# Optimization experiments

Measured on AMD Instinct MI355X. Metric: run time of the kernel, lower is better.

Reference implementation:

```python
import jax, jax.numpy as jnp
import numpy as np

D_MODEL = 1024
N_HEADS = 16
D_K = D_MODEL // N_HEADS
NEG_INF = -1.0e9


def setup_inputs() -> dict:
    key = jax.random.key(0)
    ks = jax.random.split(key, 12)
    B, S = 2, 2048
    inp = {
        "q": jax.random.normal(ks[0], (B, S, D_MODEL), dtype=jnp.float32),
        "k": jax.random.normal(ks[1], (B, S, D_MODEL), dtype=jnp.float32),
        "v": jax.random.normal(ks[2], (B, S, D_MODEL), dtype=jnp.float32),
        "mask": jax.random.randint(ks[3], (B, 1, S, S), 0, 2, dtype=jnp.int32),
        "Wq": jax.random.normal(ks[4], (D_MODEL, D_MODEL), dtype=jnp.float32) / np.sqrt(D_MODEL),
        "bq": jnp.zeros((D_MODEL,), dtype=jnp.float32),
        "Wk": jax.random.normal(ks[5], (D_MODEL, D_MODEL), dtype=jnp.float32) / np.sqrt(D_MODEL),
        "bk": jnp.zeros((D_MODEL,), dtype=jnp.float32),
        "Wv": jax.random.normal(ks[6], (D_MODEL, D_MODEL), dtype=jnp.float32) / np.sqrt(D_MODEL),
        "bv": jnp.zeros((D_MODEL,), dtype=jnp.float32),
        "Wo": jax.random.normal(ks[7], (D_MODEL, D_MODEL), dtype=jnp.float32) / np.sqrt(D_MODEL),
        "bo": jnp.zeros((D_MODEL,), dtype=jnp.float32),
    }
    return inp


def _split_heads(x):
    B, S, _ = x.shape
    return x.reshape(B, S, N_HEADS, D_K).transpose(0, 2, 1, 3)  # [B,H,S,Dk]


def reference(q, k, v, mask, Wq, bq, Wk, bk, Wv, bv, Wo, bo):
    # QKV projections (nn.Linear: x @ W.T + b; here W stored as [in,out]-agnostic square)
    query = _split_heads(q @ Wq + bq)
    key_ = _split_heads(k @ Wk + bk)
    value = _split_heads(v @ Wv + bv)

    scale = 1.0 / np.sqrt(D_K).astype(np.float32)
    scores = jnp.einsum("bhqd,bhkd->bhqk", query, key_) * scale  # [B,H,S,S]
    scores = jnp.where(mask == 0, NEG_INF, scores)
    attn = jax.nn.softmax(scores, axis=-1)  # dropout is identity in eval (p=0.0)
    ctx = jnp.einsum("bhqk,bhkd->bhqd", attn, value)  # [B,H,S,Dk]

    B, H, S, Dk = ctx.shape
    ctx = ctx.transpose(0, 2, 1, 3).reshape(B, S, H * Dk)
    return ctx @ Wo + bo
```

## Files before the change

kernel.cpp:

```cpp
#include <hip/hip_runtime.h>
#include <hip/hip_bf16.h>

typedef __bf16 bf16_t;
typedef __bf16 bf16x2 __attribute__((ext_vector_type(2)));
typedef __bf16 bf16x8 __attribute__((ext_vector_type(8)));
typedef float f32x4 __attribute__((ext_vector_type(4)));
typedef float f32x16 __attribute__((ext_vector_type(16)));
typedef int intx4 __attribute__((ext_vector_type(4)));
typedef unsigned int u32;
typedef unsigned long long u64;

#define S_LEN 2048
#define DM 1024
#define NH 16
#define DK 64
#define M_ROWS 4096
#define SCALE_LOG2E 0.1803368801111204f

__device__ __forceinline__ int sw_off(int row, int col) {
  return row * 64 + ((((col >> 3) ^ row) & 7) << 3) + (col & 7);
}

__device__ __forceinline__ bf16x8 cvt8(const float4& a, const float4& b) {
  bf16x8 v;
  v[0] = (__bf16)a.x; v[1] = (__bf16)a.y; v[2] = (__bf16)a.z; v[3] = (__bf16)a.w;
  v[4] = (__bf16)b.x; v[5] = (__bf16)b.y; v[6] = (__bf16)b.z; v[7] = (__bf16)b.w;
  return v;
}

__device__ __forceinline__ void glds16(const bf16_t* g, bf16_t* l) {
  __builtin_amdgcn_global_load_lds(
      (const __attribute__((address_space(1))) void*)g,
      (__attribute__((address_space(3))) void*)l, 16, 0, 0);
}

__device__ __forceinline__ int pk2(float lo, float hi) {
  bf16x2 t;
  t[0] = (__bf16)lo;
  t[1] = (__bf16)hi;
  return __builtin_bit_cast(int, t);
}

__global__ __launch_bounds__(256) void pack_mask(
    const int* __restrict__ mask, u64* __restrict__ mb)
{
  const int g = blockIdx.x * 256 + threadIdx.x;
  const int q = g & 2047;
  const int kw = (g >> 11) & 31;
  const int b = g >> 16;
  const int* src = &mask[((size_t)(b * S_LEN + q)) * S_LEN + kw * 64];
  u64 bits = 0;
  #pragma unroll
  for (int i = 0; i < 16; ++i) {
    const int4 m4 = *(const int4*)&src[i * 4];
    bits |= (u64)(m4.x != 0) << (4 * i);
    bits |= (u64)(m4.y != 0) << (4 * i + 1);
    bits |= (u64)(m4.z != 0) << (4 * i + 2);
    bits |= (u64)(m4.w != 0) << (4 * i + 3);
  }
  mb[g] = bits;
}

__global__ __launch_bounds__(256) void cvt_inputs(
    const float* __restrict__ q, const float* __restrict__ k,
    const float* __restrict__ v, bf16_t* __restrict__ Xb)
{
  const int z = blockIdx.y;
  const float* __restrict__ src = (z == 0) ? q : ((z == 1) ? k : v);
  const size_t idx = ((size_t)blockIdx.x * 256 + threadIdx.x) * 8;
  const float4 a = *(const float4*)&src[idx];
  const float4 b = *(const float4*)&src[idx + 4];
  *(bf16x8*)&Xb[(size_t)z * M_ROWS * DM + idx] = cvt8(a, b);
}

__global__ __launch_bounds__(256) void transw_kernel(
    const float* __restrict__ Wq, const float* __restrict__ Wk,
    const float* __restrict__ Wv, const float* __restrict__ Wo,
    bf16_t* __restrict__ Wt)
{
  const int z = blockIdx.z;
  const float* __restrict__ W = (z == 0) ? Wq : ((z == 1) ? Wk : ((z == 2) ? Wv : Wo));
  bf16_t* __restrict__ out = Wt + (size_t)z * DM * DM;
  __shared__ float tile[64][65];
  const int tx = threadIdx.x & 31, ty = threadIdx.x >> 5;
  const int k0 = blockIdx.x * 64, n0 = blockIdx.y * 64;
  #pragma unroll
  for (int j = 0; j < 8; ++j) {
    const float2 v = *(const float2*)&W[(size_t)(k0 + ty + 8 * j) * DM + n0 + tx * 2];
    tile[ty + 8 * j][tx * 2] = v.x;
    tile[ty + 8 * j][tx * 2 + 1] = v.y;
  }
  __syncthreads();
  #pragma unroll
  for (int j = 0; j < 8; ++j) {
    const int a = ty + 8 * j;
    bf16x2 p;
    p[0] = (__bf16)tile[tx * 2][a];
    p[1] = (__bf16)tile[tx * 2 + 1][a];
    *(bf16x2*)&out[(size_t)(n0 + a) * DM + k0 + tx * 2] = p;
  }
}

__device__ __forceinline__ void gemm128_body(
    const bf16_t* __restrict__ A, const bf16_t* __restrict__ Bt,
    const float* __restrict__ bias, bf16_t* __restrict__ outb,
    float* __restrict__ outf)
{
  __shared__ __align__(16) bf16_t As[128 * 32];
  __shared__ __align__(16) bf16_t Bs[128 * 32];
  const int t = threadIdx.x, w = t >> 6, L = t & 63, quad = L >> 4, l16 = L & 15;
  const int m0 = blockIdx.x * 128, n0 = blockIdx.y * 128;
  const int mb = 64 * (w & 1), nb = 64 * (w >> 1);
  const int rowS = t >> 2, subS = (t & 3) * 8;

  f32x4 acc[4][4] = {};
  for (int k0 = 0; k0 < DM; k0 += 32) {
    __syncthreads();
    glds16(&A[(size_t)(m0 + rowS) * DM + k0 + subS],        &As[t * 8]);
    glds16(&A[(size_t)(m0 + 64 + rowS) * DM + k0 + subS],   &As[2048 + t * 8]);
    glds16(&Bt[(size_t)(n0 + rowS) * DM + k0 + subS],       &Bs[t * 8]);
    glds16(&Bt[(size_t)(n0 + 64 + rowS) * DM + k0 + subS],  &Bs[2048 + t * 8]);
    __syncthreads();
    bf16x8 af[4], bfr[4];
    #pragma unroll
    for (int mt = 0; mt < 4; ++mt)
      af[mt] = *(const bf16x8*)&As[(mb + 16 * mt + l16) * 32 + quad * 8];
    #pragma unroll
    for (int ct = 0; ct < 4; ++ct)
      bfr[ct] = *(const bf16x8*)&Bs[(nb + 16 * ct + l16) * 32 + quad * 8];
    #pragma unroll
    for (int mt = 0; mt < 4; ++mt)
      #pragma unroll
      for (int ct = 0; ct < 4; ++ct)
        acc[mt][ct] = __builtin_amdgcn_mfma_f32_16x16x32_bf16(af[mt], bfr[ct], acc[mt][ct], 0, 0, 0);
  }
  #pragma unroll
  for (int mt = 0; mt < 4; ++mt)
    #pragma unroll
    for (int ct = 0; ct < 4; ++ct)
      #pragma unroll
      for (int r = 0; r < 4; ++r) {
        const int row = m0 + mb + 16 * mt + quad * 4 + r;
        const int n = n0 + nb + 16 * ct + l16;
        const float val = acc[mt][ct][r] + bias[n];
        if (outb) outb[(size_t)row * DM + n] = (__bf16)val;
        else      outf[(size_t)row * DM + n] = val;
      }
}

__global__ __launch_bounds__(256) void gemm_qkv(
    const bf16_t* __restrict__ Xb, const bf16_t* __restrict__ Wt,
    const float* __restrict__ bq, const float* __restrict__ bk,
    const float* __restrict__ bv, bf16_t* __restrict__ QKVb)
{
  const int z = blockIdx.z;
  gemm128_body(Xb + (size_t)z * M_ROWS * DM, Wt + (size_t)z * DM * DM,
               (z == 0) ? bq : ((z == 1) ? bk : bv),
               QKVb + (size_t)z * M_ROWS * DM, nullptr);
}

__global__ __launch_bounds__(256) void gemm_out(
    const bf16_t* __restrict__ ctx, const bf16_t* __restrict__ Wto,
    const float* __restrict__ bo, float* __restrict__ out)
{
  gemm128_body(ctx, Wto, bo, nullptr, out);
}

__global__ __launch_bounds__(256) void transpV(
    const bf16_t* __restrict__ Vb, bf16_t* __restrict__ Vtw)
{
  __shared__ bf16_t Tr[64 * 72];
  const int t = threadIdx.x;
  const int key0 = blockIdx.x * 64;
  const int bh = blockIdx.y, b = bh >> 4, h = bh & 15;
  const int r = t >> 2, c = (t & 3) * 16;
  const bf16_t* src = &Vb[(size_t)(b * S_LEN + key0 + r) * DM + h * DK + c];
  const bf16x8 v0 = *(const bf16x8*)src;
  const bf16x8 v1 = *(const bf16x8*)(src + 8);
  #pragma unroll
  for (int j = 0; j < 8; ++j) {
    Tr[r * 72 + c + j] = v0[j];
    Tr[r * 72 + c + 8 + j] = v1[j];
  }
  __syncthreads();
  const int dv = t >> 2, kc = (t & 3) * 16;
  bf16_t ov[16];
  #pragma unroll
  for (int j = 0; j < 16; ++j) ov[j] = Tr[(kc + j) * 72 + dv];
  bf16_t* dst = &Vtw[((size_t)bh * DK + dv) * S_LEN + key0 + kc];
  *(bf16x8*)dst = *(bf16x8*)&ov[0];
  *(bf16x8*)(dst + 8) = *(bf16x8*)&ov[8];
}

__global__ __launch_bounds__(256, 2) void attn_kernel(
    const bf16_t* __restrict__ Qb, const bf16_t* __restrict__ Kb,
    const bf16_t* __restrict__ Vtw, const u64* __restrict__ mb,
    bf16_t* __restrict__ ctx)
{
  __shared__ __align__(16) bf16_t Qs[128 * 64];
  __shared__ __align__(16) bf16_t Ks[64 * 64];
  __shared__ __align__(16) bf16_t Vts[64 * 64];

  const int t = threadIdx.x, w = t >> 6, L = t & 63;
  const int l31 = L & 31, h5 = L >> 5;
  const int q0 = blockIdx.x * 128;
  const int bh = blockIdx.y, b = bh >> 4, h = bh & 15;
  const int sr = t >> 2, sc = (t & 3) * 16;

  #pragma unroll
  for (int half = 0; half < 2; ++half) {
    const int row = half * 64 + sr;
    const bf16_t* s = &Qb[(size_t)(b * S_LEN + q0 + row) * DM + h * DK + sc];
    *(bf16x8*)&Qs[sw_off(row, sc)]     = *(const bf16x8*)s;
    *(bf16x8*)&Qs[sw_off(row, sc + 8)] = *(const bf16x8*)(s + 8);
  }

  const int qg = q0 + 32 * w + l31;
  const u64* pm = &mb[(size_t)b * 32 * S_LEN + qg];
  const bf16_t* pk_src = &Kb[(size_t)(b * S_LEN + sr) * DM + h * DK + sc];
  const bf16_t* pv_src = &Vtw[((size_t)bh * DK + sr) * S_LEN + sc];

  bf16x8 kp0, kp1, vp0, vp1;
  u64 mp;
  kp0 = *(const bf16x8*)pk_src; kp1 = *(const bf16x8*)(pk_src + 8);
  vp0 = *(const bf16x8*)pv_src; vp1 = *(const bf16x8*)(pv_src + 8);
  mp = *pm;
  pk_src += (size_t)64 * DM; pv_src += 64; pm += S_LEN;

  f32x16 O[2] = {};
  float l_lane = 0.f;

  for (int kt = 0; kt < S_LEN / 64; ++kt) {
    __syncthreads();
    *(bf16x8*)&Ks[sw_off(sr, sc)]      = kp0;
    *(bf16x8*)&Ks[sw_off(sr, sc + 8)]  = kp1;
    *(bf16x8*)&Vts[sw_off(sr, sc)]     = vp0;
    *(bf16x8*)&Vts[sw_off(sr, sc + 8)] = vp1;
    const u64 mcur = mp;
    __syncthreads();

    if (kt + 1 < S_LEN / 64) {
      kp0 = *(const bf16x8*)pk_src; kp1 = *(const bf16x8*)(pk_src + 8);
      vp0 = *(const bf16x8*)pv_src; vp1 = *(const bf16x8*)(pv_src + 8);
      mp = *pm;
      pk_src += (size_t)64 * DM; pv_src += 64; pm += S_LEN;
    }

    f32x16 sacc[2] = {};
    #pragma unroll
    for (int ks = 0; ks < 4; ++ks) {
      const bf16x8 qf = *(const bf16x8*)&Qs[sw_off(32 * w + l31, ks * 16 + 8 * h5)];
      #pragma unroll
      for (int nt = 0; nt < 2; ++nt) {
        const bf16x8 kf = *(const bf16x8*)&Ks[sw_off(nt * 32 + l31, ks * 16 + 8 * h5)];
        sacc[nt] = __builtin_amdgcn_mfma_f32_32x32x16_bf16(kf, qf, sacc[nt], 0, 0, 0);
      }
    }

    const u32 mlo = ((u32)mcur) >> (4 * h5);
    const u32 mhi = ((u32)(mcur >> 32)) >> (4 * h5);
    #pragma unroll
    for (int nt = 0; nt < 2; ++nt) {
      const u32 mm = nt ? mhi : mlo;
      float p[16];
      #pragma unroll
      for (int r = 0; r < 16; ++r) {
        const int cb = (r & 3) + 8 * (r >> 2);
        float v = __builtin_exp2f(__builtin_fmaf(sacc[nt][r], SCALE_LOG2E, -16.f));
        v = ((mm >> cb) & 1u) ? v : 0.f;
        l_lane += v;
        p[r] = v;
      }
      #pragma unroll
      for (int ss = 0; ss < 2; ++ss) {
        const int x0 = pk2(p[8 * ss + 0], p[8 * ss + 1]);
        const int x1 = pk2(p[8 * ss + 2], p[8 * ss + 3]);
        const int y0 = pk2(p[8 * ss + 4], p[8 * ss + 5]);
        const int y1 = pk2(p[8 * ss + 6], p[8 * ss + 7]);
        const auto r0 = __builtin_amdgcn_permlane32_swap(x0, y0, false, false);
        const auto r1 = __builtin_amdgcn_permlane32_swap(x1, y1, false, false);
        intx4 wv;
        wv[0] = r0[0]; wv[1] = r1[0]; wv[2] = r0[1]; wv[3] = r1[1];
        const bf16x8 pf = __builtin_bit_cast(bf16x8, wv);
        const int s4 = 2 * nt + ss;
        #pragma unroll
        for (int ot = 0; ot < 2; ++ot) {
          const bf16x8 vf = *(const bf16x8*)&Vts[sw_off(32 * ot + l31, s4 * 16 + 8 * h5)];
          O[ot] = __builtin_amdgcn_mfma_f32_32x32x16_bf16(vf, pf, O[ot], 0, 0, 0);
        }
      }
    }
  }

  const float lsum = l_lane + __shfl_xor(l_lane, 32);
  const float inv = 1.f / lsum;
  __syncthreads();
  #pragma unroll
  for (int ot = 0; ot < 2; ++ot)
    #pragma unroll
    for (int r = 0; r < 16; ++r) {
      const int dv = 32 * ot + (r & 3) + 8 * (r >> 2) + 4 * h5;
      Qs[sw_off(32 * w + l31, dv)] = (__bf16)(O[ot][r] * inv);
    }
  const int erow = 32 * w + (L >> 1);
  const int ecol = (L & 1) * 32;
  bf16_t* dst = &ctx[(size_t)(b * S_LEN + q0 + erow) * DM + h * DK + ecol];
  #pragma unroll
  for (int c8 = 0; c8 < 4; ++c8)
    *(bf16x8*)(dst + 8 * c8) = *(const bf16x8*)&Qs[sw_off(erow, ecol + 8 * c8)];
}

extern "C" void kernel_launch(void* const* d_in, const int* in_sizes, int n_in,
                              void* d_out, int out_size, void* d_ws, size_t ws_size,
                              hipStream_t stream) {
  const float* q  = (const float*)d_in[0];
  const float* k  = (const float*)d_in[1];
  const float* v  = (const float*)d_in[2];
  const int* mask = (const int*)d_in[3];
  const float* Wq = (const float*)d_in[4];
  const float* bq = (const float*)d_in[5];
  const float* Wk = (const float*)d_in[6];
  const float* bk = (const float*)d_in[7];
  const float* Wv = (const float*)d_in[8];
  const float* bv = (const float*)d_in[9];
  const float* Wo = (const float*)d_in[10];
  const float* bo = (const float*)d_in[11];
  float* out = (float*)d_out;

  const size_t SLICE = (size_t)M_ROWS * DM;
  bf16_t* Xb   = (bf16_t*)d_ws;
  bf16_t* QKVb = Xb + 3 * SLICE;
  bf16_t* Wt   = QKVb + 3 * SLICE;
  u64* mbw     = (u64*)(Wt + (size_t)4 * DM * DM);
  bf16_t* ctx  = Xb;
  bf16_t* Vtw  = Xb + SLICE;

  pack_mask<<<dim3(512), dim3(256), 0, stream>>>(mask, mbw);
  cvt_inputs<<<dim3(2048, 3), dim3(256), 0, stream>>>(q, k, v, Xb);
  transw_kernel<<<dim3(16, 16, 4), dim3(256), 0, stream>>>(Wq, Wk, Wv, Wo, Wt);
  gemm_qkv<<<dim3(32, 8, 3), dim3(256), 0, stream>>>(Xb, Wt, bq, bk, bv, QKVb);
  transpV<<<dim3(32, 32), dim3(256), 0, stream>>>(QKVb + 2 * SLICE, Vtw);
  attn_kernel<<<dim3(16, 32), dim3(256), 0, stream>>>(QKVb, QKVb + SLICE, Vtw, mbw, ctx);
  gemm_out<<<dim3(32, 8), dim3(256), 0, stream>>>(ctx, Wt + (size_t)3 * DM * DM, bo, out);
}
```

Baseline: 281.5 us.

## Double-buffer attention K/V via async LDS loads and ballot-pack the mask

The attention kernel now stages K and V tiles straight into two LDS buffers with global_load_lds, so the next tile loads while the current one is being computed. This replaces the register-prefetch path and its two barriers per tile. Q fragments are hoisted into registers once, and s_setprio raises wave priority around the MFMA sections. The mask packer now reads one element per lane in a coalesced way and builds the 64-bit word with a wave ballot, using many more blocks. The cost is extra LDS for the second buffer, which may reduce occupancy, and the code relies on the compiler placing waits for the async LDS loads before each barrier.

```diff
diff --git a/kernel.cpp b/kernel.cpp
--- a/kernel.cpp
+++ b/kernel.cpp
@@ -44,21 +44,14 @@
 __global__ __launch_bounds__(256) void pack_mask(
     const int* __restrict__ mask, u64* __restrict__ mb)
 {
-  const int g = blockIdx.x * 256 + threadIdx.x;
-  const int q = g & 2047;
-  const int kw = (g >> 11) & 31;
-  const int b = g >> 16;
-  const int* src = &mask[((size_t)(b * S_LEN + q)) * S_LEN + kw * 64];
-  u64 bits = 0;
-  #pragma unroll
-  for (int i = 0; i < 16; ++i) {
-    const int4 m4 = *(const int4*)&src[i * 4];
-    bits |= (u64)(m4.x != 0) << (4 * i);
-    bits |= (u64)(m4.y != 0) << (4 * i + 1);
-    bits |= (u64)(m4.z != 0) << (4 * i + 2);
-    bits |= (u64)(m4.w != 0) << (4 * i + 3);
-  }
-  mb[g] = bits;
+  const int wgl = blockIdx.x * 4 + (threadIdx.x >> 6);
+  const int lane = threadIdx.x & 63;
+  const int q = wgl & 2047;
+  const int kw = (wgl >> 11) & 31;
+  const int b = wgl >> 16;
+  const int val = mask[((size_t)(b * S_LEN + q)) * S_LEN + kw * 64 + lane];
+  const u64 bits = __ballot(val != 0);
+  if (lane == 0) mb[wgl] = bits;
 }
 
 __global__ __launch_bounds__(256) void cvt_inputs(
@@ -198,8 +191,8 @@
     bf16_t* __restrict__ ctx)
 {
   __shared__ __align__(16) bf16_t Qs[128 * 64];
-  __shared__ __align__(16) bf16_t Ks[64 * 64];
-  __shared__ __align__(16) bf16_t Vts[64 * 64];
+  __shared__ __align__(16) bf16_t Ks[2][64 * 64];
+  __shared__ __align__(16) bf16_t Vts[2][64 * 64];
 
   const int t = threadIdx.x, w = t >> 6, L = t & 63;
   const int l31 = L & 31, h5 = L >> 5;
@@ -214,49 +207,48 @@
     *(bf16x8*)&Qs[sw_off(row, sc)]     = *(const bf16x8*)s;
     *(bf16x8*)&Qs[sw_off(row, sc + 8)] = *(const bf16x8*)(s + 8);
   }
+  __syncthreads();
+
+  bf16x8 qf[4];
+  #pragma unroll
+  for (int ks = 0; ks < 4; ++ks)
+    qf[ks] = *(const bf16x8*)&Qs[sw_off(32 * w + l31, ks * 16 + 8 * h5)];
+
+  const int ch = (L & 7) ^ (L >> 3);
+  const int row0 = w * 16 + (L >> 3);
+  const int kofs0 = w * 1024 + L * 8, kofs1 = kofs0 + 512;
+  const bf16_t* pK0 = &Kb[(size_t)(b * S_LEN + row0) * DM + h * DK + ch * 8];
+  const bf16_t* pK1 = pK0 + (size_t)8 * DM;
+  const bf16_t* pV0 = &Vtw[((size_t)bh * DK + row0) * S_LEN + ch * 8];
+  const bf16_t* pV1 = pV0 + (size_t)8 * S_LEN;
 
   const int qg = q0 + 32 * w + l31;
   const u64* pm = &mb[(size_t)b * 32 * S_LEN + qg];
-  const bf16_t* pk_src = &Kb[(size_t)(b * S_LEN + sr) * DM + h * DK + sc];
-  const bf16_t* pv_src = &Vtw[((size_t)bh * DK + sr) * S_LEN + sc];
-
-  bf16x8 kp0, kp1, vp0, vp1;
-  u64 mp;
-  kp0 = *(const bf16x8*)pk_src; kp1 = *(const bf16x8*)(pk_src + 8);
-  vp0 = *(const bf16x8*)pv_src; vp1 = *(const bf16x8*)(pv_src + 8);
-  mp = *pm;
-  pk_src += (size_t)64 * DM; pv_src += 64; pm += S_LEN;
+
+  auto stageKV = [&](int buf) {
+    glds16(pK0, &Ks[buf][kofs0]);
+    glds16(pK1, &Ks[buf][kofs1]);
+    glds16(pV0, &Vts[buf][kofs0]);
+    glds16(pV1, &Vts[buf][kofs1]);
+    pK0 += (size_t)64 * DM; pK1 += (size_t)64 * DM;
+    pV0 += 64; pV1 += 64;
+  };
 
   f32x16 O[2] = {};
   float l_lane = 0.f;
 
-  for (int kt = 0; kt < S_LEN / 64; ++kt) {
-    __syncthreads();
-    *(bf16x8*)&Ks[sw_off(sr, sc)]      = kp0;
-    *(bf16x8*)&Ks[sw_off(sr, sc + 8)]  = kp1;
-    *(bf16x8*)&Vts[sw_off(sr, sc)]     = vp0;
-    *(bf16x8*)&Vts[sw_off(sr, sc + 8)] = vp1;
-    const u64 mcur = mp;
-    __syncthreads();
-
-    if (kt + 1 < S_LEN / 64) {
-      kp0 = *(const bf16x8*)pk_src; kp1 = *(const bf16x8*)(pk_src + 8);
-      vp0 = *(const bf16x8*)pv_src; vp1 = *(const bf16x8*)(pv_src + 8);
-      mp = *pm;
-      pk_src += (size_t)64 * DM; pv_src += 64; pm += S_LEN;
-    }
-
+  auto compute = [&](const bf16_t* __restrict__ Kc, const bf16_t* __restrict__ Vc,
+                     u64 mcur) {
     f32x16 sacc[2] = {};
-    #pragma unroll
-    for (int ks = 0; ks < 4; ++ks) {
-      const bf16x8 qf = *(const bf16x8*)&Qs[sw_off(32 * w + l31, ks * 16 + 8 * h5)];
+    __builtin_amdgcn_s_setprio(1);
+    #pragma unroll
+    for (int ks = 0; ks < 4; ++ks)
       #pragma unroll
       for (int nt = 0; nt < 2; ++nt) {
-        const bf16x8 kf = *(const bf16x8*)&Ks[sw_off(nt * 32 + l31, ks * 16 + 8 * h5)];
-        sacc[nt] = __builtin_amdgcn_mfma_f32_32x32x16_bf16(kf, qf, sacc[nt], 0, 0, 0);
+        const bf16x8 kf = *(const bf16x8*)&Kc[sw_off(nt * 32 + l31, ks * 16 + 8 * h5)];
+        sacc[nt] = __builtin_amdgcn_mfma_f32_32x32x16_bf16(kf, qf[ks], sacc[nt], 0, 0, 0);
       }
-    }
-
+    __builtin_amdgcn_s_setprio(0);
     const u32 mlo = ((u32)mcur) >> (4 * h5);
     const u32 mhi = ((u32)(mcur >> 32)) >> (4 * h5);
     #pragma unroll
@@ -283,18 +275,39 @@
         wv[0] = r0[0]; wv[1] = r1[0]; wv[2] = r0[1]; wv[3] = r1[1];
         const bf16x8 pf = __builtin_bit_cast(bf16x8, wv);
         const int s4 = 2 * nt + ss;
+        __builtin_amdgcn_s_setprio(1);
         #pragma unroll
         for (int ot = 0; ot < 2; ++ot) {
-          const bf16x8 vf = *(const bf16x8*)&Vts[sw_off(32 * ot + l31, s4 * 16 + 8 * h5)];
+          const bf16x8 vf = *(const bf16x8*)&Vc[sw_off(32 * ot + l31, s4 * 16 + 8 * h5)];
           O[ot] = __builtin_amdgcn_mfma_f32_32x32x16_bf16(vf, pf, O[ot], 0, 0, 0);
         }
+        __builtin_amdgcn_s_setprio(0);
       }
     }
+  };
+
+  stageKV(0);
+  u64 mcur = *pm; pm += S_LEN;
+  u64 mnext;
+  __syncthreads();
+
+  for (int kt = 0; kt < S_LEN / 64; kt += 2) {
+    stageKV(1);
+    mnext = *pm; pm += S_LEN;
+    compute(&Ks[0][0], &Vts[0][0], mcur);
+    __syncthreads();
+    mcur = mnext;
+    if (kt + 2 < S_LEN / 64) {
+      stageKV(0);
+      mnext = *pm; pm += S_LEN;
+    }
+    compute(&Ks[1][0], &Vts[1][0], mcur);
+    __syncthreads();
+    mcur = mnext;
   }
 
   const float lsum = l_lane + __shfl_xor(l_lane, 32);
   const float inv = 1.f / lsum;
-  __syncthreads();
   #pragma unroll
   for (int ot = 0; ot < 2; ++ot)
     #pragma unroll
@@ -335,7 +348,7 @@
   bf16_t* ctx  = Xb;
   bf16_t* Vtw  = Xb + SLICE;
 
-  pack_mask<<<dim3(512), dim3(256), 0, stream>>>(mask, mbw);
+  pack_mask<<<dim3(32768), dim3(256), 0, stream>>>(mask, mbw);
   cvt_inputs<<<dim3(2048, 3), dim3(256), 0, stream>>>(q, k, v, Xb);
   transw_kernel<<<dim3(16, 16, 4), dim3(256), 0, stream>>>(Wq, Wk, Wv, Wo, Wt);
   gemm_qkv<<<dim3(32, 8, 3), dim3(256), 0, stream>>>(Xb, Wt, bq, bk, bv, QKVb);
```

Result: no change. 286.8 us (+1.9%).
